# Performance work log

Hardware: AMD Instinct MI355X
Metric: run time of the kernel (lower is better)

The kernel has to match this reference:

```python
import jax, jax.numpy as jnp
import numpy as np

B, T, C, H = 2, 2048, 1024, 16
HD = C // H  # 64
EPS = 1e-5


def _ln(x, g, b):
    mu = jnp.mean(x, axis=-1, keepdims=True)
    var = jnp.var(x, axis=-1, keepdims=True)
    return (x - mu) * jax.lax.rsqrt(var + EPS) * g + b


def setup_inputs() -> dict:
    key = jax.random.key(0)
    ks = jax.random.split(key, 8)
    s = lambda n: 1.0 / np.sqrt(n)
    return {
        "x": jax.random.normal(ks[0], (B, T, C), dtype=jnp.float32),
        "ln1_g": jnp.ones((C,), jnp.float32), "ln1_b": jnp.zeros((C,), jnp.float32),
        "ln2_g": jnp.ones((C,), jnp.float32), "ln2_b": jnp.zeros((C,), jnp.float32),
        "w_in": jax.random.normal(ks[1], (C, 3 * C), jnp.float32) * s(C),
        "b_in": jnp.zeros((3 * C,), jnp.float32),
        "w_out": jax.random.normal(ks[2], (C, C), jnp.float32) * s(C),
        "b_out": jnp.zeros((C,), jnp.float32),
        "w_fc": jax.random.normal(ks[3], (C, 4 * C), jnp.float32) * s(C),
        "b_fc": jnp.zeros((4 * C,), jnp.float32),
        "w_proj": jax.random.normal(ks[4], (4 * C, C), jnp.float32) * s(4 * C),
        "b_proj": jnp.zeros((C,), jnp.float32),
    }


def reference(x, ln1_g, ln1_b, ln2_g, ln2_b, w_in, b_in, w_out, b_out,
              w_fc, b_fc, w_proj, b_proj):
    # --- residual 1: x + attn(ln1(x)) ---
    h = _ln(x, ln1_g, ln1_b)
    qkv = h @ w_in + b_in                          # (B,T,3C)
    # reshape to (B,T,H,3*HD) then chunk per head (matches torch code exactly)
    qkv = qkv.reshape(B, T, H, 3 * HD).transpose(0, 2, 1, 3)  # (B,H,T,3*HD)
    q, k, v = jnp.split(qkv, 3, axis=-1)           # each (B,H,T,HD)
    att = jnp.einsum('bhqd,bhkd->bhqk', q, k) / np.sqrt(HD)
    causal = jnp.tril(jnp.ones((T, T), bool))
    att = jnp.where(causal, att, -jnp.inf)
    att = jax.nn.softmax(att, axis=-1)
    o = jnp.einsum('bhqk,bhkd->bhqd', att, v)      # (B,H,T,HD)
    o = o.transpose(0, 2, 1, 3).reshape(B, T, C)
    x1 = x + (o @ w_out + b_out)
    # --- ln2 applied to residual stream, then residual 2 on top of ln2 output ---
    y = _ln(x1, ln2_g, ln2_b)
    mlp = jax.nn.gelu(y @ w_fc + b_fc, approximate=False) @ w_proj + b_proj
    return y + mlp
```

## Files before the change

### kernel.cpp

```cpp
#include <hip/hip_runtime.h>
#include <hip/hip_bf16.h>
#include <math.h>

typedef __bf16 bf16;
typedef __bf16 bf16x8 __attribute__((ext_vector_type(8)));
typedef __bf16 bf16x4 __attribute__((ext_vector_type(4)));
typedef float floatx4 __attribute__((ext_vector_type(4)));

#define B_ 2
#define T_ 2048
#define C_ 1024
#define H_ 16
#define HD_ 64


__device__ __forceinline__ void gload_lds16(const bf16* g, bf16* l) {
    __builtin_amdgcn_global_load_lds(
        (const __attribute__((address_space(1))) unsigned int*)(g),
        (__attribute__((address_space(3))) unsigned int*)(l), 16, 0, 0);
}

__global__ __launch_bounds__(256) void transpose_all(
        const float* __restrict__ w_in, const float* __restrict__ w_out,
        const float* __restrict__ w_fc, const float* __restrict__ w_proj,
        bf16* __restrict__ o_in, bf16* __restrict__ o_out,
        bf16* __restrict__ o_fc, bf16* __restrict__ o_proj) {
    __shared__ float shf[64 * 33];
    int t = blockIdx.x;
    int tid = threadIdx.x;
    if (t < 7168) {
        const float* src; bf16* dst; int K, N, idx;
        if (t < 3072) { src = w_in; dst = o_in; K = 1024; N = 3072; idx = t; }
        else          { src = w_fc; dst = o_fc; K = 1024; N = 4096; idx = t - 3072; }
        int ntx = N >> 5;
        int nt = (idx % ntx) * 32, kt = (idx / ntx) * 32;
        int tx = tid & 31, ty = tid >> 5;
        #pragma unroll
        for (int i = 0; i < 32; i += 8)
            shf[(ty + i) * 33 + tx] = src[(size_t)(kt + ty + i) * N + nt + tx];
        __syncthreads();
        #pragma unroll
        for (int i = 0; i < 32; i += 8)
            dst[(size_t)(nt + ty + i) * K + kt + tx] = (bf16)shf[tx * 33 + ty + i];
    } else {
        const float* src; bf16* dst; int K, idx;
        if (t < 7680) { src = w_out;  dst = o_out;  K = 1024; idx = t - 7168; }
        else          { src = w_proj; dst = o_proj; K = 4096; idx = t - 7680; }
        const int N = 1024;
        int n0 = (idx & 31) * 32, k0 = (idx >> 5) * 64;
        int col = tid & 31, kr = tid >> 5;
        #pragma unroll
        for (int s = 0; s < 8; s++)
            shf[(kr + s * 8) * 33 + col] = src[(size_t)(k0 + kr + s * 8) * N + n0 + col];
        __syncthreads();
        int tl = tid >> 6, l = tid & 63;
        int ntl = tl & 1, kcl = tl >> 1;
        int rr = ntl * 16 + (l & 15);
        int qd = l >> 4;
        bf16x8 v;
        #pragma unroll
        for (int e = 0; e < 8; e++)
            v[e] = (bf16)shf[(kcl * 32 + qd * 8 + e) * 33 + rr];
        size_t nt_g = (n0 >> 4) + ntl, kc_g = (k0 >> 5) + kcl;
        *(bf16x8*)(dst + (nt_g * (K >> 5) + kc_g) * 512 + l * 8) = v;
    }
}

__global__ __launch_bounds__(256) void ln_kernel(const float* __restrict__ x,
                                                 const float* __restrict__ g,
                                                 const float* __restrict__ b,
                                                 bf16* __restrict__ out_b,
                                                 float* __restrict__ out_f) {
    int row = blockIdx.x;
    int tid = threadIdx.x;
    const float* xr = x + (size_t)row * C_;
    float4 v = ((const float4*)xr)[tid];
    float s  = v.x + v.y + v.z + v.w;
    float ss = v.x * v.x + v.y * v.y + v.z * v.z + v.w * v.w;
    #pragma unroll
    for (int off = 32; off; off >>= 1) {
        s  += __shfl_down(s, off);
        ss += __shfl_down(ss, off);
    }
    __shared__ float red[8];
    int wid = tid >> 6;
    if ((tid & 63) == 0) { red[wid] = s; red[wid + 4] = ss; }
    __syncthreads();
    s  = red[0] + red[1] + red[2] + red[3];
    ss = red[4] + red[5] + red[6] + red[7];
    float mean = s * (1.0f / C_);
    float var  = ss * (1.0f / C_) - mean * mean;
    float rstd = rsqrtf(var + 1e-5f);
    float4 gv = ((const float4*)g)[tid];
    float4 bv = ((const float4*)b)[tid];
    float o0 = (v.x - mean) * rstd * gv.x + bv.x;
    float o1 = (v.y - mean) * rstd * gv.y + bv.y;
    float o2 = (v.z - mean) * rstd * gv.z + bv.z;
    float o3 = (v.w - mean) * rstd * gv.w + bv.w;
    bf16x4 ob = { (bf16)o0, (bf16)o1, (bf16)o2, (bf16)o3 };
    ((bf16x4*)out_b)[(size_t)row * 256 + tid] = ob;
    if (out_f) {
        float4 of; of.x = o0; of.y = o1; of.z = o2; of.w = o3;
        ((float4*)out_f)[(size_t)row * 256 + tid] = of;
    }
}

__device__ __forceinline__ float gelu_exact(float v) {
    return 0.5f * v * (1.0f + erff(v * 0.70710678118654752f));
}

template<int MODE>
__global__ __launch_bounds__(256) void gemm128(const bf16* __restrict__ A,
                                               const bf16* __restrict__ Bt,
                                               const float* __restrict__ bias,
                                               void* __restrict__ out,
                                               int M, int N, int K) {
    __shared__ __align__(16) bf16 smem[128 * 136];
    bf16* As = smem;
    bf16* Bs = smem + 128 * 64;

    int m0 = blockIdx.y * 128, n0 = blockIdx.x * 128;
    int tid = threadIdx.x;
    int wid = __builtin_amdgcn_readfirstlane(tid >> 6);
    int lane = tid & 63;
    int lm = lane & 15, quad = lane >> 4;
    int wm = (wid & 1) * 64;
    int wn = (wid >> 1) * 64;
    int lrow = lane >> 3;
    int lcol = (lane & 7) * 8;

    const bf16* Ablk = A  + (size_t)m0 * K;
    const bf16* Bblk = Bt + (size_t)n0 * K;

    floatx4 acc[4][4];
    #pragma unroll
    for (int i = 0; i < 4; i++)
        #pragma unroll
        for (int j = 0; j < 4; j++) { floatx4 z = {0.f, 0.f, 0.f, 0.f}; acc[i][j] = z; }

    for (int k0 = 0; k0 < K; k0 += 64) {
        __syncthreads();
        #pragma unroll
        for (int c = 0; c < 4; c++) {
            int row = wid * 32 + c * 8;
            gload_lds16(Ablk + (size_t)(row + lrow) * K + k0 + lcol, As + row * 64);
        }
        #pragma unroll
        for (int c = 0; c < 4; c++) {
            int row = wid * 32 + c * 8;
            gload_lds16(Bblk + (size_t)(row + lrow) * K + k0 + lcol, Bs + row * 64);
        }
        __syncthreads();
        #pragma unroll
        for (int kc = 0; kc < 2; kc++) {
            bf16x8 af[4], bfr[4];
            #pragma unroll
            for (int i = 0; i < 4; i++)
                af[i] = *(const bf16x8*)(As + (wm + i * 16 + lm) * 64 + kc * 32 + quad * 8);
            #pragma unroll
            for (int j = 0; j < 4; j++)
                bfr[j] = *(const bf16x8*)(Bs + (wn + j * 16 + lm) * 64 + kc * 32 + quad * 8);
            #pragma unroll
            for (int i = 0; i < 4; i++)
                #pragma unroll
                for (int j = 0; j < 4; j++)
                    acc[i][j] = __builtin_amdgcn_mfma_f32_16x16x32_bf16(af[i], bfr[j], acc[i][j], 0, 0, 0);
        }
    }

    if (MODE == 0) {
        #pragma unroll
        for (int i = 0; i < 4; i++)
            #pragma unroll
            for (int j = 0; j < 4; j++) {
                int mbase = m0 + wm + i * 16 + quad * 4;
                int n     = n0 + wn + j * 16 + lm;
                float bsn = bias[n];
                #pragma unroll
                for (int r = 0; r < 4; r++)
                    ((bf16*)out)[(size_t)(mbase + r) * N + n] = (bf16)(acc[i][j][r] + bsn);
            }
    } else {
        __syncthreads();
        #pragma unroll
        for (int i = 0; i < 4; i++)
            #pragma unroll
            for (int j = 0; j < 4; j++) {
                int n = n0 + wn + j * 16 + lm;
                float bsn = bias[n];
                #pragma unroll
                for (int r = 0; r < 4; r++)
                    smem[(wm + i * 16 + quad * 4 + r) * 136 + wn + j * 16 + lm] =
                        (bf16)gelu_exact(acc[i][j][r] + bsn);
            }
        __syncthreads();
        bf16* ob = (bf16*)out;
        int kcb = n0 >> 5;
        #pragma unroll
        for (int p = 0; p < 8; p++) {
            int tl = wid * 8 + p;
            int mtl = tl >> 2, kcl = tl & 3;
            bf16x8 v = *(const bf16x8*)&smem[(mtl * 16 + lm) * 136 + kcl * 32 + quad * 8];
            *(bf16x8*)(ob + (((size_t)((m0 >> 4) + mtl) * (N >> 5) + kcb + kcl) * 512) + lane * 8) = v;
        }
    }
}

__global__ __launch_bounds__(256) void gemm_direct(const bf16* __restrict__ Af,
                                                   const bf16* __restrict__ Bf,
                                                   const float* __restrict__ bias,
                                                   const float* __restrict__ add,
                                                   float* __restrict__ out,
                                                   int M, int N, int K) {
    int lin = blockIdx.x;
    int xcd = lin & 7, loc = lin >> 3;
    int m0 = ((xcd << 2) | (loc & 3)) * 128;
    int n0 = (loc >> 2) * 64;
    int tid = threadIdx.x;
    int wid = __builtin_amdgcn_readfirstlane(tid >> 6);
    int lane = tid & 63;
    int lm = lane & 15, quad = lane >> 4;
    int wm = (wid & 1) * 64, wn = (wid >> 1) * 32;
    int KC = K >> 5;
    const bf16* Ab = Af + ((size_t)((m0 + wm) >> 4) * KC) * 512 + lane * 8;
    const bf16* Bb = Bf + ((size_t)((n0 + wn) >> 4) * KC) * 512 + lane * 8;

    floatx4 acc[4][2];
    #pragma unroll
    for (int i = 0; i < 4; i++)
        #pragma unroll
        for (int j = 0; j < 2; j++) { floatx4 z = {0.f, 0.f, 0.f, 0.f}; acc[i][j] = z; }

    bf16x8 ac[4][2], bc[2][2], an[4][2], bn[2][2];
    #pragma unroll
    for (int i = 0; i < 4; i++)
        #pragma unroll
        for (int c = 0; c < 2; c++)
            ac[i][c] = *(const bf16x8*)(Ab + ((size_t)i * KC + c) * 512);
    #pragma unroll
    for (int j = 0; j < 2; j++)
        #pragma unroll
        for (int c = 0; c < 2; c++)
            bc[j][c] = *(const bf16x8*)(Bb + ((size_t)j * KC + c) * 512);

    for (int kc0 = 0; kc0 < KC; kc0 += 2) {
        bool pre = (kc0 + 2) < KC;
        if (pre) {
            #pragma unroll
            for (int i = 0; i < 4; i++)
                #pragma unroll
                for (int c = 0; c < 2; c++)
                    an[i][c] = *(const bf16x8*)(Ab + ((size_t)i * KC + kc0 + 2 + c) * 512);
            #pragma unroll
            for (int j = 0; j < 2; j++)
                #pragma unroll
                for (int c = 0; c < 2; c++)
                    bn[j][c] = *(const bf16x8*)(Bb + ((size_t)j * KC + kc0 + 2 + c) * 512);
        }
        #pragma unroll
        for (int c = 0; c < 2; c++)
            #pragma unroll
            for (int i = 0; i < 4; i++)
                #pragma unroll
                for (int j = 0; j < 2; j++)
                    acc[i][j] = __builtin_amdgcn_mfma_f32_16x16x32_bf16(ac[i][c], bc[j][c], acc[i][j], 0, 0, 0);
        if (pre) {
            #pragma unroll
            for (int i = 0; i < 4; i++)
                #pragma unroll
                for (int c = 0; c < 2; c++) ac[i][c] = an[i][c];
            #pragma unroll
            for (int j = 0; j < 2; j++)
                #pragma unroll
                for (int c = 0; c < 2; c++) bc[j][c] = bn[j][c];
        }
    }

    #pragma unroll
    for (int i = 0; i < 4; i++)
        #pragma unroll
        for (int j = 0; j < 2; j++) {
            int mbase = m0 + wm + i * 16 + quad * 4;
            int n     = n0 + wn + j * 16 + lm;
            float bsn = bias[n];
            #pragma unroll
            for (int r = 0; r < 4; r++) {
                size_t idx = (size_t)(mbase + r) * N + n;
                out[idx] = acc[i][j][r] + bsn + add[idx];
            }
        }
}

#define QT_ 128
#define KT_ 64

__global__ __launch_bounds__(256) void attn_mfma_kernel(const bf16* __restrict__ qkv,
                                                        bf16* __restrict__ of) {
    int bh = blockIdx.x;
    int b = bh >> 4, h = bh & 15;
    int q0 = (gridDim.y - 1 - blockIdx.y) * QT_;
    int tid = threadIdx.x, wid = tid >> 6, lane = tid & 63;
    int wm = wid * 32;
    int lm = lane & 15, quad = lane >> 4;
    int sw = lm & 7;

    const bf16* base = qkv + (size_t)b * T_ * (3 * C_) + h * (3 * HD_);

    __shared__ __align__(16) bf16 Ks[KT_][72];
    __shared__ __align__(16) bf16 Vt[HD_][72];
    __shared__ __align__(16) bf16 PsT[4][32][64];

    bf16x8 qf[2][2];
    #pragma unroll
    for (int am = 0; am < 2; am++)
        #pragma unroll
        for (int kc = 0; kc < 2; kc++) {
            int r = q0 + wm + am * 16 + lm;
            qf[am][kc] = *(const bf16x8*)(base + (size_t)r * (3 * C_) + kc * 32 + quad * 8);
        }

    floatx4 acc_o[2][4];
    #pragma unroll
    for (int am = 0; am < 2; am++)
        #pragma unroll
        for (int dn = 0; dn < 4; dn++) { floatx4 z = {0.f, 0.f, 0.f, 0.f}; acc_o[am][dn] = z; }
    float mst[2] = { -1e30f, -1e30f };
    float lst[2] = { 0.0f, 0.0f };

    int scol = (tid & 7) * 8;

    int kmax = q0 + QT_;
    for (int k0 = 0; k0 < kmax; k0 += KT_) {
        int kr0 = tid >> 3;
        bf16x8 kv0 = *(const bf16x8*)(base + (size_t)(k0 + kr0)      * (3 * C_) + HD_ + scol);
        bf16x8 kv1 = *(const bf16x8*)(base + (size_t)(k0 + kr0 + 32) * (3 * C_) + HD_ + scol);
        bf16x8 vv0 = *(const bf16x8*)(base + (size_t)(k0 + kr0)      * (3 * C_) + 2 * HD_ + scol);
        bf16x8 vv1 = *(const bf16x8*)(base + (size_t)(k0 + kr0 + 32) * (3 * C_) + 2 * HD_ + scol);
        __syncthreads();
        *(bf16x8*)(&Ks[kr0][scol])      = kv0;
        *(bf16x8*)(&Ks[kr0 + 32][scol]) = kv1;
        {
            int c = scol >> 3;
            int pk0 = (((kr0)       >> 3) ^ c) * 8 + (kr0 & 7);
            int pk1 = (((kr0 + 32)  >> 3) ^ c) * 8 + (kr0 & 7);
            #pragma unroll
            for (int j = 0; j < 8; j++) {
                Vt[scol + j][pk0] = vv0[j];
                Vt[scol + j][pk1] = vv1[j];
            }
        }
        __syncthreads();

        if (k0 <= q0 + wm + 31) {
            floatx4 st[4][2];
            #pragma unroll
            for (int bn = 0; bn < 4; bn++)
                #pragma unroll
                for (int am = 0; am < 2; am++) { floatx4 z = {0.f, 0.f, 0.f, 0.f}; st[bn][am] = z; }
            #pragma unroll
            for (int kc = 0; kc < 2; kc++) {
                bf16x8 kf[4];
                #pragma unroll
                for (int bn = 0; bn < 4; bn++)
                    kf[bn] = *(const bf16x8*)(&Ks[bn * 16 + lm][kc * 32 + quad * 8]);
                #pragma unroll
                for (int bn = 0; bn < 4; bn++)
                    #pragma unroll
                    for (int am = 0; am < 2; am++)
                        st[bn][am] = __builtin_amdgcn_mfma_f32_16x16x32_bf16(kf[bn], qf[am][kc], st[bn][am], 0, 0, 0);
            }

            float alpha_s[2];
            #pragma unroll
            for (int am = 0; am < 2; am++) {
                int gq = q0 + wm + am * 16 + lm;
                int need_mask = (k0 + KT_ - 1) > (q0 + wm + am * 16);
                float vv[4][4];
                float rm = -1e30f;
                #pragma unroll
                for (int bn = 0; bn < 4; bn++)
                    #pragma unroll
                    for (int r = 0; r < 4; r++) {
                        float sv = st[bn][am][r] * 0.125f;
                        int key = k0 + bn * 16 + quad * 4 + r;
                        sv = (!need_mask || key <= gq) ? sv : -1e30f;
                        vv[bn][r] = sv;
                        rm = fmaxf(rm, sv);
                    }
                rm = fmaxf(rm, __shfl_xor(rm, 16));
                rm = fmaxf(rm, __shfl_xor(rm, 32));
                float mold = mst[am];
                float mnew = fmaxf(mold, rm);
                float alpha = __expf(mold - mnew);
                mst[am] = mnew;
                float ps = 0.f;
                #pragma unroll
                for (int bn = 0; bn < 4; bn++) {
                    float p0 = __expf(vv[bn][0] - mnew);
                    float p1 = __expf(vv[bn][1] - mnew);
                    float p2 = __expf(vv[bn][2] - mnew);
                    float p3 = __expf(vv[bn][3] - mnew);
                    ps += (p0 + p1) + (p2 + p3);
                    bf16x4 pk = { (bf16)p0, (bf16)p1, (bf16)p2, (bf16)p3 };
                    int kb = bn * 2 + (quad >> 1);
                    int col = ((kb ^ sw) << 3) + (quad & 1) * 4;
                    *(bf16x4*)(&PsT[wid][am * 16 + lm][col]) = pk;
                }
                ps += __shfl_xor(ps, 16);
                ps += __shfl_xor(ps, 32);
                lst[am] = lst[am] * alpha + ps;
                alpha_s[am] = alpha;
            }

            #pragma unroll
            for (int am = 0; am < 2; am++)
                #pragma unroll
                for (int r = 0; r < 4; r++) {
                    float ar = __shfl(alpha_s[am], quad * 4 + r);
                    #pragma unroll
                    for (int dn = 0; dn < 4; dn++) acc_o[am][dn][r] *= ar;
                }

            __asm__ volatile("s_waitcnt lgkmcnt(0)" ::: "memory");

            #pragma unroll
            for (int kc = 0; kc < 2; kc++) {
                bf16x8 pa[2], vfr[4];
                #pragma unroll
                for (int am = 0; am < 2; am++)
                    pa[am] = *(const bf16x8*)(&PsT[wid][am * 16 + lm][((kc * 4 + quad) ^ sw) << 3]);
                #pragma unroll
                for (int dn = 0; dn < 4; dn++) {
                    int d = dn * 16 + lm;
                    int swd = (d >> 3) & 7;
                    vfr[dn] = *(const bf16x8*)(&Vt[d][(((kc * 4 + quad) ^ swd) << 3)]);
                }
                #pragma unroll
                for (int am = 0; am < 2; am++)
                    #pragma unroll
                    for (int dn = 0; dn < 4; dn++)
                        acc_o[am][dn] = __builtin_amdgcn_mfma_f32_16x16x32_bf16(pa[am], vfr[dn], acc_o[am][dn], 0, 0, 0);
            }
        }
    }

    #pragma unroll
    for (int am = 0; am < 2; am++) {
        float il = 1.0f / lst[am];
        #pragma unroll
        for (int r = 0; r < 4; r++) {
            float ir = __shfl(il, quad * 4 + r);
            #pragma unroll
            for (int dn = 0; dn < 4; dn++)
                PsT[wid][am * 16 + quad * 4 + r][dn * 16 + lm] = (bf16)(acc_o[am][dn][r] * ir);
        }
    }
    __asm__ volatile("s_waitcnt lgkmcnt(0)" ::: "memory");
    size_t mtb = ((size_t)b * T_ + q0 + wm) >> 4;
    #pragma unroll
    for (int am = 0; am < 2; am++)
        #pragma unroll
        for (int kcl = 0; kcl < 2; kcl++) {
            bf16x8 v = *(const bf16x8*)&PsT[wid][am * 16 + lm][kcl * 32 + quad * 8];
            *(bf16x8*)(of + ((mtb + am) * (C_ >> 5) + (h * 2 + kcl)) * 512 + lane * 8) = v;
        }
}

extern "C" void kernel_launch(void* const* d_in, const int* in_sizes, int n_in,
                              void* d_out, int out_size, void* d_ws, size_t ws_size,
                              hipStream_t stream) {
    (void)in_sizes; (void)n_in; (void)out_size; (void)ws_size;
    const float* x      = (const float*)d_in[0];
    const float* ln1_g  = (const float*)d_in[1];
    const float* ln1_b  = (const float*)d_in[2];
    const float* ln2_g  = (const float*)d_in[3];
    const float* ln2_b  = (const float*)d_in[4];
    const float* w_in   = (const float*)d_in[5];
    const float* b_in   = (const float*)d_in[6];
    const float* w_out  = (const float*)d_in[7];
    const float* b_out  = (const float*)d_in[8];
    const float* w_fc   = (const float*)d_in[9];
    const float* b_fc   = (const float*)d_in[10];
    const float* w_proj = (const float*)d_in[11];
    const float* b_proj = (const float*)d_in[12];

    char* ws = (char*)d_ws;
    const size_t MB = 1024 * 1024;
    bf16*  w_inT   = (bf16*)(ws + 0);
    bf16*  w_outF  = (bf16*)(ws + 6 * MB);
    bf16*  w_fcT   = (bf16*)(ws + 8 * MB);
    bf16*  w_projF = (bf16*)(ws + 16 * MB);
    bf16*  qkv     = (bf16*)(ws + 24 * MB);
    bf16*  fc_frag = (bf16*)(ws + 24 * MB);
    bf16*  o_frag  = (bf16*)(ws + 56 * MB);
    bf16*  y_b     = (bf16*)(ws + 56 * MB);
    bf16*  h_b     = (bf16*)(ws + 64 * MB);
    float* x1      = (float*)(ws + 64 * MB);
    float* y_f     = (float*)(ws + 80 * MB);

    const int M = B_ * T_;

    transpose_all<<<9728, 256, 0, stream>>>(w_in, w_out, w_fc, w_proj,
                                            w_inT, w_outF, w_fcT, w_projF);

    ln_kernel<<<M, 256, 0, stream>>>(x, ln1_g, ln1_b, h_b, nullptr);
    gemm128<0><<<dim3(3 * C_ / 128, M / 128), 256, 0, stream>>>(h_b, w_inT, b_in,
                                                                qkv, M, 3 * C_, C_);
    attn_mfma_kernel<<<dim3(B_ * H_, T_ / QT_), 256, 0, stream>>>(qkv, o_frag);
    gemm_direct<<<512, 256, 0, stream>>>(o_frag, w_outF, b_out, x, x1, M, C_, C_);
    ln_kernel<<<M, 256, 0, stream>>>(x1, ln2_g, ln2_b, y_b, y_f);
    gemm128<1><<<dim3(4 * C_ / 128, M / 128), 256, 0, stream>>>(y_b, w_fcT, b_fc,
                                                                fc_frag, M, 4 * C_, C_);
    gemm_direct<<<512, 256, 0, stream>>>(fc_frag, w_projF, b_proj, y_f,
                                         (float*)d_out, M, C_, 4 * C_);
}
```

Baseline: 373.9 us.

## Split attention query tile across 8 waves of 16 rows each

The attention kernel now launches 512 threads per block, so each of 8 waves owns 16 query rows instead of 4 waves owning 32. Each thread also loads one K/V row per tile instead of two. The softmax scale is folded into Q at load time, and the mask is applied only on diagonal tiles, avoiding per-element multiply and compare elsewhere. This is meant to raise parallelism and latency hiding for the same 128-row query tile and reduce per-wave register pressure. The cost is that each K/V tile is reused by fewer rows per wave, and pre-scaling Q in bf16 adds a small rounding difference.

```diff
diff --git a/kernel.cpp b/kernel.cpp
--- a/kernel.cpp
+++ b/kernel.cpp
@@ -294,69 +294,57 @@
 #define QT_ 128
 #define KT_ 64
 
-__global__ __launch_bounds__(256) void attn_mfma_kernel(const bf16* __restrict__ qkv,
+__global__ __launch_bounds__(512) void attn_mfma_kernel(const bf16* __restrict__ qkv,
                                                         bf16* __restrict__ of) {
     int bh = blockIdx.x;
     int b = bh >> 4, h = bh & 15;
     int q0 = (gridDim.y - 1 - blockIdx.y) * QT_;
     int tid = threadIdx.x, wid = tid >> 6, lane = tid & 63;
-    int wm = wid * 32;
     int lm = lane & 15, quad = lane >> 4;
     int sw = lm & 7;
+    int r0 = q0 + wid * 16;
 
     const bf16* base = qkv + (size_t)b * T_ * (3 * C_) + h * (3 * HD_);
 
     __shared__ __align__(16) bf16 Ks[KT_][72];
     __shared__ __align__(16) bf16 Vt[HD_][72];
-    __shared__ __align__(16) bf16 PsT[4][32][64];
-
-    bf16x8 qf[2][2];
-    #pragma unroll
-    for (int am = 0; am < 2; am++)
-        #pragma unroll
-        for (int kc = 0; kc < 2; kc++) {
-            int r = q0 + wm + am * 16 + lm;
-            qf[am][kc] = *(const bf16x8*)(base + (size_t)r * (3 * C_) + kc * 32 + quad * 8);
-        }
-
-    floatx4 acc_o[2][4];
-    #pragma unroll
-    for (int am = 0; am < 2; am++)
-        #pragma unroll
-        for (int dn = 0; dn < 4; dn++) { floatx4 z = {0.f, 0.f, 0.f, 0.f}; acc_o[am][dn] = z; }
-    float mst[2] = { -1e30f, -1e30f };
-    float lst[2] = { 0.0f, 0.0f };
-
+    __shared__ __align__(16) bf16 PsT[8][16][64];
+
+    bf16x8 qf[2];
+    #pragma unroll
+    for (int kc = 0; kc < 2; kc++) {
+        bf16x8 t = *(const bf16x8*)(base + (size_t)(r0 + lm) * (3 * C_) + kc * 32 + quad * 8);
+        #pragma unroll
+        for (int e = 0; e < 8; e++) t[e] = (bf16)((float)t[e] * 0.125f);
+        qf[kc] = t;
+    }
+
+    floatx4 acc_o[4];
+    #pragma unroll
+    for (int dn = 0; dn < 4; dn++) { floatx4 z = {0.f, 0.f, 0.f, 0.f}; acc_o[dn] = z; }
+    float mst = -1e30f, lst = 0.0f;
+
+    int srow = tid >> 3;
     int scol = (tid & 7) * 8;
 
     int kmax = q0 + QT_;
     for (int k0 = 0; k0 < kmax; k0 += KT_) {
-        int kr0 = tid >> 3;
-        bf16x8 kv0 = *(const bf16x8*)(base + (size_t)(k0 + kr0)      * (3 * C_) + HD_ + scol);
-        bf16x8 kv1 = *(const bf16x8*)(base + (size_t)(k0 + kr0 + 32) * (3 * C_) + HD_ + scol);
-        bf16x8 vv0 = *(const bf16x8*)(base + (size_t)(k0 + kr0)      * (3 * C_) + 2 * HD_ + scol);
-        bf16x8 vv1 = *(const bf16x8*)(base + (size_t)(k0 + kr0 + 32) * (3 * C_) + 2 * HD_ + scol);
-        __syncthreads();
-        *(bf16x8*)(&Ks[kr0][scol])      = kv0;
-        *(bf16x8*)(&Ks[kr0 + 32][scol]) = kv1;
+        bf16x8 kv = *(const bf16x8*)(base + (size_t)(k0 + srow) * (3 * C_) + HD_ + scol);
+        bf16x8 vv = *(const bf16x8*)(base + (size_t)(k0 + srow) * (3 * C_) + 2 * HD_ + scol);
+        __syncthreads();
+        *(bf16x8*)(&Ks[srow][scol]) = kv;
         {
             int c = scol >> 3;
-            int pk0 = (((kr0)       >> 3) ^ c) * 8 + (kr0 & 7);
-            int pk1 = (((kr0 + 32)  >> 3) ^ c) * 8 + (kr0 & 7);
-            #pragma unroll
-            for (int j = 0; j < 8; j++) {
-                Vt[scol + j][pk0] = vv0[j];
-                Vt[scol + j][pk1] = vv1[j];
-            }
-        }
-        __syncthreads();
-
-        if (k0 <= q0 + wm + 31) {
-            floatx4 st[4][2];
-            #pragma unroll
-            for (int bn = 0; bn < 4; bn++)
-                #pragma unroll
-                for (int am = 0; am < 2; am++) { floatx4 z = {0.f, 0.f, 0.f, 0.f}; st[bn][am] = z; }
+            int pk = ((srow >> 3) ^ c) * 8 + (srow & 7);
+            #pragma unroll
+            for (int j = 0; j < 8; j++) Vt[scol + j][pk] = vv[j];
+        }
+        __syncthreads();
+
+        if (k0 <= r0 + 15) {
+            floatx4 st[4];
+            #pragma unroll
+            for (int bn = 0; bn < 4; bn++) { floatx4 z = {0.f, 0.f, 0.f, 0.f}; st[bn] = z; }
             #pragma unroll
             for (int kc = 0; kc < 2; kc++) {
                 bf16x8 kf[4];
@@ -365,70 +353,66 @@
                     kf[bn] = *(const bf16x8*)(&Ks[bn * 16 + lm][kc * 32 + quad * 8]);
                 #pragma unroll
                 for (int bn = 0; bn < 4; bn++)
-                    #pragma unroll
-                    for (int am = 0; am < 2; am++)
-                        st[bn][am] = __builtin_amdgcn_mfma_f32_16x16x32_bf16(kf[bn], qf[am][kc], st[bn][am], 0, 0, 0);
-            }
-
-            float alpha_s[2];
-            #pragma unroll
-            for (int am = 0; am < 2; am++) {
-                int gq = q0 + wm + am * 16 + lm;
-                int need_mask = (k0 + KT_ - 1) > (q0 + wm + am * 16);
-                float vv[4][4];
-                float rm = -1e30f;
+                    st[bn] = __builtin_amdgcn_mfma_f32_16x16x32_bf16(kf[bn], qf[kc], st[bn], 0, 0, 0);
+            }
+
+            float vv_[4][4];
+            float rm = -1e30f;
+            if (k0 + KT_ - 1 > r0) {
+                int gq = r0 + lm;
                 #pragma unroll
                 for (int bn = 0; bn < 4; bn++)
                     #pragma unroll
                     for (int r = 0; r < 4; r++) {
-                        float sv = st[bn][am][r] * 0.125f;
                         int key = k0 + bn * 16 + quad * 4 + r;
-                        sv = (!need_mask || key <= gq) ? sv : -1e30f;
-                        vv[bn][r] = sv;
+                        float sv = (key <= gq) ? st[bn][r] : -1e30f;
+                        vv_[bn][r] = sv;
                         rm = fmaxf(rm, sv);
                     }
-                rm = fmaxf(rm, __shfl_xor(rm, 16));
-                rm = fmaxf(rm, __shfl_xor(rm, 32));
-                float mold = mst[am];
-                float mnew = fmaxf(mold, rm);
-                float alpha = __expf(mold - mnew);
-                mst[am] = mnew;
-                float ps = 0.f;
-                #pragma unroll
-                for (int bn = 0; bn < 4; bn++) {
-                    float p0 = __expf(vv[bn][0] - mnew);
-                    float p1 = __expf(vv[bn][1] - mnew);
-                    float p2 = __expf(vv[bn][2] - mnew);
-                    float p3 = __expf(vv[bn][3] - mnew);
-                    ps += (p0 + p1) + (p2 + p3);
-                    bf16x4 pk = { (bf16)p0, (bf16)p1, (bf16)p2, (bf16)p3 };
-                    int kb = bn * 2 + (quad >> 1);
-                    int col = ((kb ^ sw) << 3) + (quad & 1) * 4;
-                    *(bf16x4*)(&PsT[wid][am * 16 + lm][col]) = pk;
-                }
-                ps += __shfl_xor(ps, 16);
-                ps += __shfl_xor(ps, 32);
-                lst[am] = lst[am] * alpha + ps;
-                alpha_s[am] = alpha;
-            }
-
-            #pragma unroll
-            for (int am = 0; am < 2; am++)
-                #pragma unroll
-                for (int r = 0; r < 4; r++) {
-                    float ar = __shfl(alpha_s[am], quad * 4 + r);
+            } else {
+                #pragma unroll
+                for (int bn = 0; bn < 4; bn++)
                     #pragma unroll
-                    for (int dn = 0; dn < 4; dn++) acc_o[am][dn][r] *= ar;
-                }
+                    for (int r = 0; r < 4; r++) {
+                        vv_[bn][r] = st[bn][r];
+                        rm = fmaxf(rm, st[bn][r]);
+                    }
+            }
+            rm = fmaxf(rm, __shfl_xor(rm, 16));
+            rm = fmaxf(rm, __shfl_xor(rm, 32));
+            float mnew = fmaxf(mst, rm);
+            float alpha = __expf(mst - mnew);
+            mst = mnew;
+            float ps = 0.f;
+            #pragma unroll
+            for (int bn = 0; bn < 4; bn++) {
+                float p0 = __expf(vv_[bn][0] - mnew);
+                float p1 = __expf(vv_[bn][1] - mnew);
+                float p2 = __expf(vv_[bn][2] - mnew);
+                float p3 = __expf(vv_[bn][3] - mnew);
+                ps += (p0 + p1) + (p2 + p3);
+                bf16x4 pk = { (bf16)p0, (bf16)p1, (bf16)p2, (bf16)p3 };
+                int kb = bn * 2 + (quad >> 1);
+                int col = ((kb ^ sw) << 3) + (quad & 1) * 4;
+                *(bf16x4*)(&PsT[wid][lm][col]) = pk;
+            }
+            ps += __shfl_xor(ps, 16);
+            ps += __shfl_xor(ps, 32);
+            lst = lst * alpha + ps;
+
+            #pragma unroll
+            for (int r = 0; r < 4; r++) {
+                float ar = __shfl(alpha, quad * 4 + r);
+                #pragma unroll
+                for (int dn = 0; dn < 4; dn++) acc_o[dn][r] *= ar;
+            }
 
             __asm__ volatile("s_waitcnt lgkmcnt(0)" ::: "memory");
 
             #pragma unroll
             for (int kc = 0; kc < 2; kc++) {
-                bf16x8 pa[2], vfr[4];
-                #pragma unroll
-                for (int am = 0; am < 2; am++)
-                    pa[am] = *(const bf16x8*)(&PsT[wid][am * 16 + lm][((kc * 4 + quad) ^ sw) << 3]);
+                bf16x8 pa = *(const bf16x8*)(&PsT[wid][lm][((kc * 4 + quad) ^ sw) << 3]);
+                bf16x8 vfr[4];
                 #pragma unroll
                 for (int dn = 0; dn < 4; dn++) {
                     int d = dn * 16 + lm;
@@ -436,34 +420,27 @@
                     vfr[dn] = *(const bf16x8*)(&Vt[d][(((kc * 4 + quad) ^ swd) << 3)]);
                 }
                 #pragma unroll
-                for (int am = 0; am < 2; am++)
-                    #pragma unroll
-                    for (int dn = 0; dn < 4; dn++)
-                        acc_o[am][dn] = __builtin_amdgcn_mfma_f32_16x16x32_bf16(pa[am], vfr[dn], acc_o[am][dn], 0, 0, 0);
-            }
-        }
-    }
-
-    #pragma unroll
-    for (int am = 0; am < 2; am++) {
-        float il = 1.0f / lst[am];
-        #pragma unroll
-        for (int r = 0; r < 4; r++) {
-            float ir = __shfl(il, quad * 4 + r);
-            #pragma unroll
-            for (int dn = 0; dn < 4; dn++)
-                PsT[wid][am * 16 + quad * 4 + r][dn * 16 + lm] = (bf16)(acc_o[am][dn][r] * ir);
-        }
+                for (int dn = 0; dn < 4; dn++)
+                    acc_o[dn] = __builtin_amdgcn_mfma_f32_16x16x32_bf16(pa, vfr[dn], acc_o[dn], 0, 0, 0);
+            }
+        }
+    }
+
+    float il = 1.0f / lst;
+    #pragma unroll
+    for (int r = 0; r < 4; r++) {
+        float ir = __shfl(il, quad * 4 + r);
+        #pragma unroll
+        for (int dn = 0; dn < 4; dn++)
+            PsT[wid][quad * 4 + r][dn * 16 + lm] = (bf16)(acc_o[dn][r] * ir);
     }
     __asm__ volatile("s_waitcnt lgkmcnt(0)" ::: "memory");
-    size_t mtb = ((size_t)b * T_ + q0 + wm) >> 4;
-    #pragma unroll
-    for (int am = 0; am < 2; am++)
-        #pragma unroll
-        for (int kcl = 0; kcl < 2; kcl++) {
-            bf16x8 v = *(const bf16x8*)&PsT[wid][am * 16 + lm][kcl * 32 + quad * 8];
-            *(bf16x8*)(of + ((mtb + am) * (C_ >> 5) + (h * 2 + kcl)) * 512 + lane * 8) = v;
-        }
+    size_t mtb = ((size_t)b * T_ + r0) >> 4;
+    #pragma unroll
+    for (int kcl = 0; kcl < 2; kcl++) {
+        bf16x8 v = *(const bf16x8*)&PsT[wid][lm][kcl * 32 + quad * 8];
+        *(bf16x8*)(of + (mtb * (C_ >> 5) + (h * 2 + kcl)) * 512 + lane * 8) = v;
+    }
 }
 
 extern "C" void kernel_launch(void* const* d_in, const int* in_sizes, int n_in,
@@ -506,7 +483,7 @@
     ln_kernel<<<M, 256, 0, stream>>>(x, ln1_g, ln1_b, h_b, nullptr);
     gemm128<0><<<dim3(3 * C_ / 128, M / 128), 256, 0, stream>>>(h_b, w_inT, b_in,
                                                                 qkv, M, 3 * C_, C_);
-    attn_mfma_kernel<<<dim3(B_ * H_, T_ / QT_), 256, 0, stream>>>(qkv, o_frag);
+    attn_mfma_kernel<<<dim3(B_ * H_, T_ / QT_), 512, 0, stream>>>(qkv, o_frag);
     gemm_direct<<<512, 256, 0, stream>>>(o_frag, w_outF, b_out, x, x1, M, C_, C_);
     ln_kernel<<<M, 256, 0, stream>>>(x1, ln2_g, ln2_b, y_b, y_f);
     gemm128<1><<<dim3(4 * C_ / 128, M / 128), 256, 0, stream>>>(y_b, w_fcT, b_fc,
```

Measured after the change: 354.4 us. 1.05x faster.
